# Kernel optimization log

Hardware: AMD Instinct MI355X
Metric: run time of the kernel (lower is better)

## Reference

```python
import jax, jax.numpy as jnp
import numpy as np

# dims
B, CIN, COUT, H, W, K = 4, 64, 64, 128, 128, 9
DM, DS, DC, DI, DTR = K, 16, 4, 2 * K, 1  # mamba: d_model, d_state, d_conv, d_inner, dt_rank=ceil(9/16)
EXTEND_SCOPE = 1.0


def silu(x):
    return x * jax.nn.sigmoid(x)


def conv2d(x, w, b, stride, pad):
    y = jax.lax.conv_general_dilated(x, w, stride, pad, dimension_numbers=("NCHW", "OIHW", "NCHW"))
    return y + b[None, :, None, None]


def group_norm(x, g, b, groups, eps=1e-5):
    Bb, C, Hh, Ww = x.shape
    xg = x.reshape(Bb, groups, C // groups, Hh, Ww)
    mu = xg.mean(axis=(2, 3, 4), keepdims=True)
    var = ((xg - mu) ** 2).mean(axis=(2, 3, 4), keepdims=True)
    xn = ((xg - mu) * jax.lax.rsqrt(var + eps)).reshape(Bb, C, Hh, Ww)
    return xn * g[None, :, None, None] + b[None, :, None, None]


def trc_flatten(x):
    # two-row columnwise interleave flatten; [B,C,Hh,Ww] -> [B,C,Hh*Ww] (Hh even here)
    Bb, Cc, Hh, Ww = x.shape
    return x.reshape(Bb, Cc, Hh // 2, 2, Ww).transpose(0, 1, 2, 4, 3).reshape(Bb, Cc, Hh * Ww)


def trc_inverse(xf, Hh, Ww):
    Bb, Cc, _ = xf.shape
    return xf.reshape(Bb, Cc, Hh // 2, Ww, 2).transpose(0, 1, 2, 4, 3).reshape(Bb, Cc, Hh, Ww)


def mamba(xs, in_proj_w, conv1d_w, conv1d_b, x_proj_w, dt_proj_w, dt_proj_b, A_log, D_p, out_proj_w):
    # standard selective-scan Mamba block; xs: [B,L,DM]
    Bb, L, _ = xs.shape
    xz = xs @ in_proj_w.T                      # [B,L,2*DI]
    xi, z = jnp.split(xz, 2, axis=-1)
    xc = jnp.pad(xi.transpose(0, 2, 1), ((0, 0), (0, 0), (DC - 1, 0)))  # causal pad
    xc = jax.lax.conv_general_dilated(xc, conv1d_w, (1,), "VALID", feature_group_count=DI,
                                      dimension_numbers=("NCH", "OIH", "NCH")) + conv1d_b[None, :, None]
    xi = silu(xc.transpose(0, 2, 1))           # [B,L,DI]
    dbl = xi @ x_proj_w.T
    dt = dbl[..., :DTR]
    Bs = dbl[..., DTR:DTR + DS]
    Cs = dbl[..., DTR + DS:]
    dt = jax.nn.softplus(dt @ dt_proj_w.T + dt_proj_b)  # [B,L,DI]
    A = -jnp.exp(A_log)                        # [DI,DS]
    dA = jnp.exp(dt[..., None] * A)            # [B,L,DI,DS]
    dBx = dt[..., None] * Bs[:, :, None, :] * xi[..., None]

    def step(h, inp):
        da, dbx, c = inp
        h = da * h + dbx
        return h, jnp.einsum("bds,bs->bd", h, c)

    h0 = jnp.zeros((Bb, DI, DS), xs.dtype)
    _, ys = jax.lax.scan(step, h0, (dA.transpose(1, 0, 2, 3), dBx.transpose(1, 0, 2, 3), Cs.transpose(1, 0, 2)))
    y = ys.transpose(1, 0, 2) + D_p * xi
    y = y * silu(z)
    return y @ out_proj_w.T


def bilinear_sample(feat, py, px):
    # feat [B,C,Hf,Wf]; py,px pixel coords [B,Ho,Wo] (already clamped in-range)
    Hf, Wf = feat.shape[-2:]
    y0 = jnp.floor(py)
    x0 = jnp.floor(px)
    wy = (py - y0)[:, None]
    wx = (px - x0)[:, None]
    y0i = jnp.clip(y0.astype(jnp.int32), 0, Hf - 1)
    y1i = jnp.clip(y0i + 1, 0, Hf - 1)
    x0i = jnp.clip(x0.astype(jnp.int32), 0, Wf - 1)
    x1i = jnp.clip(x0i + 1, 0, Wf - 1)
    g = jax.vmap(lambda f, yi, xi: f[:, yi, xi])
    v00 = g(feat, y0i, x0i)
    v01 = g(feat, y0i, x1i)
    v10 = g(feat, y1i, x0i)
    v11 = g(feat, y1i, x1i)
    return v00 * (1 - wy) * (1 - wx) + v01 * (1 - wy) * wx + v10 * wy * (1 - wx) + v11 * wy * wx


def setup_inputs() -> dict:
    key = jax.random.key(0)
    ks = jax.random.split(key, 20)
    r = lambda i, shape, s: jax.random.normal(ks[i], shape, dtype=jnp.float32) * s
    return {
        "x": jax.random.normal(ks[0], (B, CIN, H, W), dtype=jnp.float32),
        "offset_w": r(1, (2 * K, CIN, 3, 3), 0.05),
        "offset_b": jnp.zeros((2 * K,), jnp.float32),
        "gno_g": jnp.ones((2 * K,), jnp.float32),
        "gno_b": jnp.zeros((2 * K,), jnp.float32),
        "altho": jnp.array(np.log(np.e - 1.0), jnp.float32),
        "in_proj_w": r(2, (2 * DI, DM), 0.2),
        "conv1d_w": r(3, (DI, 1, DC), 0.2),
        "conv1d_b": jnp.zeros((DI,), jnp.float32),
        "x_proj_w": r(4, (DTR + 2 * DS, DI), 0.2),
        "dt_proj_w": r(5, (DI, DTR), 0.2),
        "dt_proj_b": r(6, (DI,), 0.2),
        "A_log": jnp.log(jnp.broadcast_to(jnp.arange(1, DS + 1, dtype=jnp.float32), (DI, DS))),
        "D_p": jnp.ones((DI,), jnp.float32),
        "out_proj_w": r(7, (DM, DI), 0.2),
        "dsc_w": r(8, (COUT, CIN, K, 1), 0.05),
        "dsc_b": jnp.zeros((COUT,), jnp.float32),
        "gn_g": jnp.ones((COUT,), jnp.float32),
        "gn_b": jnp.zeros((COUT,), jnp.float32),
    }


def reference(x, offset_w, offset_b, gno_g, gno_b, altho, in_proj_w, conv1d_w, conv1d_b,
              x_proj_w, dt_proj_w, dt_proj_b, A_log, D_p, out_proj_w, dsc_w, dsc_b, gn_g, gn_b):
    off = conv2d(x, offset_w, offset_b, (1, 1), [(1, 1), (1, 1)])      # [B,2K,W,H]
    off = jnp.tanh(group_norm(off, gno_g, gno_b, K))
    y_off = off[:, :K]                                                  # [B,K,W,H]
    center = K // 2
    Wc, Hc = y_off.shape[2], y_off.shape[3]

    # sequential offset accumulation away from the center row (center stays 0)
    rows = [None] * K
    rows[center] = jnp.zeros_like(y_off[:, 0])
    for i in range(1, center + 1):
        rows[center + i] = rows[center + i - 1] + y_off[:, center + i]
        rows[center - i] = rows[center - i + 1] + y_off[:, center - i]
    y_cum = jnp.stack(rows, axis=1)                                     # [B,K,W,H]

    y_center = jnp.arange(Wc, dtype=jnp.float32)[None, None, :, None]
    x_center = jnp.arange(Hc, dtype=jnp.float32)[None, None, None, :]
    x_spread = jnp.linspace(-center, center, K, dtype=jnp.float32)[None, :, None, None]
    y_new = y_center + y_cum * EXTEND_SCOPE                             # y_spread is zeros
    x_new = jnp.broadcast_to(x_center + x_spread, (B, K, Wc, Hc))

    # Mamba selective scan over the two-row columnwise flattened offsets
    y_seq = trc_flatten(y_off).transpose(0, 2, 1)                       # [B, Wc*Hc, K]
    y_m = mamba(y_seq, in_proj_w, conv1d_w, conv1d_b, x_proj_w, dt_proj_w, dt_proj_b, A_log, D_p, out_proj_w)
    y_keep = trc_inverse(y_m.transpose(0, 2, 1), Wc, Hc)                # [B,K,W,H]

    wgt = jnp.maximum(jax.nn.softplus(altho), 0.01)
    y = wgt * y_keep + y_new

    y_map = y.transpose(0, 2, 1, 3).reshape(B, Wc * K, Hc)              # b (w k) h
    x_map = x_new.transpose(0, 2, 1, 3).reshape(B, Wc * K, Hc)

    py = jnp.clip(y_map, 0.0, H - 1)
    px = jnp.clip(x_map, 0.0, W - 1)
    deformed = bilinear_sample(x, py, px)                               # [B,CIN,W*K,H]

    out = conv2d(deformed, dsc_w, dsc_b, (K, 1), "VALID")               # [B,COUT,W,H]
    out = group_norm(out, gn_g, gn_b, COUT // 4)
    return out
```

## Files before the change

### kernel.cpp

```cpp
#include <hip/hip_runtime.h>
#include <math.h>

#define BB 4
#define HH 128
#define WW 128
#define HW (HH*WW)
#define LSEQ HW
#define NCH 1024
#define CLEN 16

typedef _Float16 half8 __attribute__((ext_vector_type(8)));
typedef float floatx4 __attribute__((ext_vector_type(4)));
typedef float floatx16 __attribute__((ext_vector_type(16)));

constexpr size_t OFF_RAW_O = 0;
constexpr size_t OFF_RAW_N = (size_t)BB*10*HW;
constexpr size_t YSEQT_O = OFF_RAW_O + OFF_RAW_N;
constexpr size_t YSEQT_N = (size_t)BB*9*LSEQ;
constexpr size_t YNEW_O = YSEQT_O + YSEQT_N;
constexpr size_t YNEW_N = (size_t)BB*9*HW;
constexpr size_t GN1_O = YNEW_O + YNEW_N;
constexpr size_t GN1_N = 64;
constexpr size_t CH18 = (size_t)BB*18*LSEQ;
constexpr size_t CH16 = (size_t)BB*16*LSEQ;
constexpr size_t DT_O = GN1_O + GN1_N;
constexpr size_t XI_O = DT_O + CH18;
constexpr size_t ZZ_O = XI_O + CH18;
constexpr size_t BS_O = ZZ_O + CH18;
constexpr size_t CS_O = BS_O + CH16;
constexpr size_t CARR = (size_t)BB*NCH*288;
constexpr size_t CP_O = CS_O + CH16;
constexpr size_t CHC_O = CP_O + CARR;
constexpr size_t HIN_O = CHC_O + CARR;
constexpr size_t YS_O = HIN_O + CARR;
constexpr size_t YFIN_O = YS_O + CH18;
constexpr size_t XTH_O = YFIN_O + YNEW_N;
constexpr size_t XTH_N = (size_t)BB*HW*32;
constexpr size_t XTL_O = XTH_O + XTH_N;
constexpr size_t OUTPRE_O = XTL_O + XTH_N;
constexpr size_t OUTPRE_N = (size_t)BB*64*HW;
constexpr size_t WT_O = OUTPRE_O + OUTPRE_N;
constexpr size_t AO_O = WT_O + 36864;
constexpr size_t AMAT_O = AO_O + 9216;
constexpr size_t GN2_O = AMAT_O + 288;
constexpr size_t WS_TOTAL = GN2_O + 128;

__global__ void prep_kernel(const float* __restrict__ dsc_w, const float* __restrict__ offw,
                            const float* __restrict__ A_log,
                            _Float16* __restrict__ AH, _Float16* __restrict__ AL,
                            _Float16* __restrict__ AOH, _Float16* __restrict__ AOL,
                            float* __restrict__ Amat,
                            float* __restrict__ gn1s, float* __restrict__ gn2s){
  int i = blockIdx.x*blockDim.x + threadIdx.x;
  if(blockIdx.x==0){
    if(threadIdx.x<40) gn1s[threadIdx.x]=0.f;
    if(threadIdx.x>=64 && threadIdx.x<192) gn2s[threadIdx.x-64]=0.f;
  }
  if(i < 36864){
    int jj = i&7, gg = (i>>3)&1, co = (i>>4)&63, ks = i>>10;
    int k = ks>>2, q = ks&3;
    int ci = q*16 + gg*8 + jj;
    float w = dsc_w[((size_t)(co*64 + ci))*9 + k];
    _Float16 h = (_Float16)w;
    AH[i] = h;
    AL[i] = (_Float16)(w - (float)h);
  }
  int j = i - 36864;
  if(j >= 0 && j < 9216){
    int jj = j&7, lane = (j>>3)&63, ksl = j>>9;
    int tap = ksl>>1, ks = ksl&1;
    int co = lane&15, kg = lane>>4;
    int ci = ks*32 + kg*8 + jj;
    int dy = tap/3, dx = tap%3;
    float w = (co<10) ? offw[((size_t)(co*64 + ci)*3 + dy)*3 + dx] : 0.f;
    _Float16 h = (_Float16)w;
    AOH[j] = h;
    AOL[j] = (_Float16)(w - (float)h);
  }
  int a = i - 46080;
  if(a >= 0 && a < 288) Amat[a] = -__expf(A_log[a]);
}

__global__ __launch_bounds__(256) void transpose_x_kernel(const float* __restrict__ x,
                                                          _Float16* __restrict__ xTh,
                                                          _Float16* __restrict__ xTl){
  __shared__ float tile[64][65];
  int blk = blockIdx.x;
  int w0 = (blk&1)*64;
  int h  = (blk>>1)&127;
  int b  = blk>>8;
  int lane = threadIdx.x&63, q = threadIdx.x>>6;
  #pragma unroll
  for(int r=0;r<16;r++){
    int ci = r*4 + q;
    tile[ci][lane] = x[((size_t)(b*64+ci)*HH + h)*WW + w0 + lane];
  }
  __syncthreads();
  #pragma unroll
  for(int r=0;r<16;r++){
    int w = r*4 + q;
    float v = tile[lane][w];
    size_t o = (((size_t)(b*HH+h))*WW + w0 + w)*64 + lane;
    _Float16 hv = (_Float16)v;
    xTh[o] = hv;
    xTl[o] = (_Float16)(v - (float)hv);
  }
}

__global__ __launch_bounds__(256) void off_conv_kernel(
    const _Float16* __restrict__ xTh,
    const _Float16* __restrict__ AOH, const _Float16* __restrict__ AOL,
    const float* __restrict__ offb, float* __restrict__ off_raw,
    float* __restrict__ gn1sums){
  __shared__ float sred[6][2];
  int blk0 = blockIdx.x;
  int blk = (blk0&7)*64 + (blk0>>3);
  int h = blk&127, b = blk>>7;
  int lane = threadIdx.x&63, wv = threadIdx.x>>6;
  int col = lane&15, kg = lane>>4;
  if(threadIdx.x<10) ((float*)sred)[threadIdx.x]=0.f;
  __syncthreads();
  floatx4 acc[2];
  acc[0] = (floatx4)0.f; acc[1] = (floatx4)0.f;
  for(int dy=0; dy<3; dy++){
    int hr = h + dy - 1;
    if(hr < 0 || hr >= HH) continue;
    for(int dx=0; dx<3; dx++){
      int tap = dy*3 + dx;
      #pragma unroll
      for(int ks=0; ks<2; ks++){
        half8 ah = *(const half8*)(AOH + (size_t)((tap*2+ks)*64 + lane)*8);
        half8 al = *(const half8*)(AOL + (size_t)((tap*2+ks)*64 + lane)*8);
        #pragma unroll
        for(int tt=0; tt<2; tt++){
          int px = wv*32 + tt*16 + col;
          int wc = px + dx - 1;
          half8 bh = {};
          if(wc >= 0 && wc < WW)
            bh = *(const half8*)(xTh + (((size_t)(b*HH+hr))*WW + wc)*64 + ks*32 + kg*8);
          acc[tt] = __builtin_amdgcn_mfma_f32_16x16x32_f16(ah, bh, acc[tt], 0,0,0);
          acc[tt] = __builtin_amdgcn_mfma_f32_16x16x32_f16(al, bh, acc[tt], 0,0,0);
        }
      }
    }
  }
  float gs[2][2] = {{0.f,0.f},{0.f,0.f}};
  #pragma unroll
  for(int tt=0; tt<2; tt++){
    #pragma unroll
    for(int r=0; r<4; r++){
      int co = kg*4 + r;
      if(co < 10){
        int px = wv*32 + tt*16 + col;
        float v = acc[tt][r] + offb[co];
        off_raw[((size_t)(b*10+co)*HH + h)*WW + px] = v;
        gs[r>>1][0] += v; gs[r>>1][1] += v*v;
      }
    }
  }
  #pragma unroll
  for(int m=1;m<16;m<<=1){
    gs[0][0]+=__shfl_xor(gs[0][0],m,16); gs[0][1]+=__shfl_xor(gs[0][1],m,16);
    gs[1][0]+=__shfl_xor(gs[1][0],m,16); gs[1][1]+=__shfl_xor(gs[1][1],m,16);
  }
  if((lane&15)==0){
    int g0 = kg*2;
    if(g0<5){ atomicAdd(&sred[g0][0],gs[0][0]); atomicAdd(&sred[g0][1],gs[0][1]); }
    if(g0+1<5){ atomicAdd(&sred[g0+1][0],gs[1][0]); atomicAdd(&sred[g0+1][1],gs[1][1]); }
  }
  __syncthreads();
  if(threadIdx.x<10) atomicAdd(&gn1sums[b*10+threadIdx.x], ((float*)sred)[threadIdx.x]);
}

__global__ __launch_bounds__(256) void gn1_apply_kernel(const float* __restrict__ off_raw,
                                                        const float* __restrict__ gn1sums,
                                                        const float* __restrict__ gno_g,
                                                        const float* __restrict__ gno_b,
                                                        float* __restrict__ yseqT,
                                                        float* __restrict__ ynew){
  int idx = blockIdx.x*blockDim.x + threadIdx.x;
  int b = idx>>14; int pix = idx&16383; int h = pix>>7, w = pix&127;
  float t[9];
  #pragma unroll
  for(int c=0;c<9;c++){
    float v = off_raw[((size_t)(b*10+c))*HW + pix];
    int gi = b*10 + (c>>1)*2;
    float S = gn1sums[gi], S2 = gn1sums[gi+1];
    float mu = S*(1.f/32768.f);
    float inv = rsqrtf(S2*(1.f/32768.f) - mu*mu + 1e-5f);
    float xx = (v-mu)*inv*gno_g[c] + gno_b[c];
    xx = fminf(fmaxf(xx,-15.f),15.f);
    float e2 = __expf(2.f*xx);
    t[c] = (e2-1.f)/(e2+1.f);
  }
  int l = (((h>>1)*WW + w)<<1) | (h&1);
  #pragma unroll
  for(int c=0;c<9;c++) yseqT[((size_t)(b*9+c))*LSEQ + l] = t[c];
  float rows[9];
  rows[4]=0.f;
  rows[5]=t[5]; rows[6]=rows[5]+t[6]; rows[7]=rows[6]+t[7]; rows[8]=rows[7]+t[8];
  rows[3]=t[3]; rows[2]=rows[3]+t[2]; rows[1]=rows[2]+t[1]; rows[0]=rows[1]+t[0];
  #pragma unroll
  for(int k=0;k<9;k++) ynew[((size_t)(b*9+k))*HW + pix] = (float)h + rows[k];
}

__global__ __launch_bounds__(256) void mamba_feat_kernel(
    const float* __restrict__ yseqT, const float* __restrict__ in_proj_w,
    const float* __restrict__ conv_w, const float* __restrict__ conv_b,
    const float* __restrict__ x_proj_w, const float* __restrict__ dt_w,
    const float* __restrict__ dt_b,
    float* __restrict__ DT_L, float* __restrict__ XI_L, float* __restrict__ ZZ_L,
    float* __restrict__ BS_L, float* __restrict__ CS_L){
  __shared__ float s_in[36*9], s_cw[18*4], s_cb[18], s_xw[33*18], s_dw[18], s_db[18];
  for(int i=threadIdx.x;i<324;i+=256) s_in[i]=in_proj_w[i];
  for(int i=threadIdx.x;i<72;i+=256)  s_cw[i]=conv_w[i];
  for(int i=threadIdx.x;i<594;i+=256) s_xw[i]=x_proj_w[i];
  if(threadIdx.x<18){ s_cb[threadIdx.x]=conv_b[threadIdx.x];
                      s_dw[threadIdx.x]=dt_w[threadIdx.x];
                      s_db[threadIdx.x]=dt_b[threadIdx.x]; }
  __syncthreads();
  int idx = blockIdx.x*blockDim.x + threadIdx.x;
  int b = idx>>14, l = idx&16383;
  float ys4[4][9];
  #pragma unroll
  for(int m=0;m<9;m++){
    const float* p = yseqT + (size_t)(b*9+m)*LSEQ;
    #pragma unroll
    for(int t=0;t<4;t++){
      int lp = l-3+t;
      ys4[t][m] = (lp>=0) ? p[lp] : 0.f;
    }
  }
  float xi[18];
  #pragma unroll
  for(int d=0;d<18;d++){
    float cacc = s_cb[d];
    #pragma unroll
    for(int t=0;t<4;t++){
      float xr = 0.f;
      #pragma unroll
      for(int m=0;m<9;m++) xr += ys4[t][m]*s_in[d*9+m];
      cacc += xr * s_cw[d*4+t];
    }
    xi[d] = cacc / (1.f + __expf(-cacc));
  }
  float dblv[33];
  #pragma unroll
  for(int j=0;j<33;j++){
    float a=0.f;
    #pragma unroll
    for(int d=0;d<18;d++) a += xi[d]*s_xw[j*18+d];
    dblv[j]=a;
  }
  size_t lb = (size_t)b*LSEQ + l;
  #pragma unroll
  for(int d=0;d<18;d++) XI_L[lb*18 + d] = xi[d];
  #pragma unroll
  for(int d=0;d<18;d++){
    float a=0.f;
    #pragma unroll
    for(int m=0;m<9;m++) a += ys4[3][m]*s_in[(18+d)*9+m];
    ZZ_L[lb*18 + d] = a;
    float pre = dblv[0]*s_dw[d] + s_db[d];
    DT_L[lb*18 + d] = fmaxf(pre,0.f) + __logf(1.f + __expf(-fabsf(pre)));
  }
  #pragma unroll
  for(int s=0;s<16;s++){
    BS_L[lb*16 + s] = dblv[1+s];
    CS_L[lb*16 + s] = dblv[17+s];
  }
}

__global__ __launch_bounds__(288) void scan_pass1(const float* __restrict__ DT_L,
                                                  const float* __restrict__ XI_L,
                                                  const float* __restrict__ BS_L,
                                                  const float* __restrict__ Amat,
                                                  float* __restrict__ CP, float* __restrict__ CH){
  __shared__ float tile[16][18][17];
  int blk = blockIdx.x;
  int b = blk>>6; int ckb = (blk&63)<<4;
  int tid = threadIdx.x;
  int d = tid%18, ck = tid/18;
  int c = ckb + ck;
  int l0 = c*CLEN;
  float A[16];
  #pragma unroll
  for(int i=0;i<4;i++){
    float4 t = *(const float4*)(Amat + d*16 + i*4);
    A[i*4]=t.x; A[i*4+1]=t.y; A[i*4+2]=t.z; A[i*4+3]=t.w;
  }
  float h[16], P[16];
  #pragma unroll
  for(int s=0;s<16;s++){ h[s]=0.f; P[s]=1.f; }
  const float* dtp = DT_L + ((size_t)b*LSEQ + l0)*18 + d;
  const float* xip = XI_L + ((size_t)b*LSEQ + l0)*18 + d;
  const float* bsp = BS_L + ((size_t)b*LSEQ + l0)*16;
  #pragma unroll 4
  for(int st=0; st<CLEN; ++st){
    float dt  = dtp[st*18];
    float dx  = dt*xip[st*18];
    float Bv[16];
    #pragma unroll
    for(int i=0;i<4;i++){
      float4 t = *(const float4*)(bsp + st*16 + i*4);
      Bv[i*4]=t.x; Bv[i*4+1]=t.y; Bv[i*4+2]=t.z; Bv[i*4+3]=t.w;
    }
    #pragma unroll
    for(int s=0;s<16;s++){
      float a = __expf(dt*A[s]);
      h[s] = a*h[s] + dx*Bv[s];
      P[s] *= a;
    }
  }
  #pragma unroll
  for(int s=0;s<16;s++) tile[s][d][ck] = P[s];
  __syncthreads();
  {
    int t = tid; int d2 = t>>4, s2 = t&15;
    float* dst = CP + ((size_t)(b*288 + t))*NCH + ckb;
    const float* src = &tile[s2][d2][0];
    #pragma unroll
    for(int i=0;i<4;i++) ((float4*)dst)[i] = *(const float4*)(src + i*4);
  }
  __syncthreads();
  #pragma unroll
  for(int s=0;s<16;s++) tile[s][d][ck] = h[s];
  __syncthreads();
  {
    int t = tid; int d2 = t>>4, s2 = t&15;
    float* dst = CH + ((size_t)(b*288 + t))*NCH + ckb;
    const float* src = &tile[s2][d2][0];
    #pragma unroll
    for(int i=0;i<4;i++) ((float4*)dst)[i] = *(const float4*)(src + i*4);
  }
}

__global__ __launch_bounds__(256) void scan_carry_kernel(const float* __restrict__ CP,
                                                         const float* __restrict__ CH,
                                                         float* __restrict__ HIN){
  int wid = blockIdx.x*4 + (threadIdx.x>>6);
  int lane = threadIdx.x&63;
  int b = wid/288, t = wid%288;
  size_t base = ((size_t)(b*288 + t))*NCH;
  int c0 = lane*16;
  float P[16], Hh[16];
  #pragma unroll
  for(int i=0;i<4;i++){
    float4 tp = *(const float4*)(CP + base + c0 + i*4);
    float4 th = *(const float4*)(CH + base + c0 + i*4);
    P[i*4]=tp.x; P[i*4+1]=tp.y; P[i*4+2]=tp.z; P[i*4+3]=tp.w;
    Hh[i*4]=th.x; Hh[i*4+1]=th.y; Hh[i*4+2]=th.z; Hh[i*4+3]=th.w;
  }
  float aP = P[0], aH = Hh[0];
  #pragma unroll
  for(int i=1;i<16;i++){ aH = P[i]*aH + Hh[i]; aP = aP*P[i]; }
  float sP = aP, sH = aH;
  #pragma unroll
  for(int off=1; off<64; off<<=1){
    float pP = __shfl_up(sP, off, 64);
    float pH = __shfl_up(sH, off, 64);
    if(lane >= off){ sH = sP*pH + sH; sP = pP*sP; }
  }
  float eH = __shfl_up(sH, 1, 64);
  if(lane==0){ eH=0.f; }
  float cHh = eH;
  float outv[16];
  #pragma unroll
  for(int i=0;i<16;i++){
    outv[i] = cHh;
    cHh = P[i]*cHh + Hh[i];
  }
  #pragma unroll
  for(int i=0;i<4;i++){
    float4 tv; tv.x=outv[i*4]; tv.y=outv[i*4+1]; tv.z=outv[i*4+2]; tv.w=outv[i*4+3];
    *(float4*)(HIN + base + c0 + i*4) = tv;
  }
}

__global__ __launch_bounds__(288) void scan_pass2(const float* __restrict__ DT_L,
                                                  const float* __restrict__ XI_L,
                                                  const float* __restrict__ BS_L,
                                                  const float* __restrict__ CS_L,
                                                  const float* __restrict__ Amat,
                                                  const float* __restrict__ HIN,
                                                  float* __restrict__ YST_L){
  __shared__ float tile[16][18][17];
  int blk = blockIdx.x;
  int b = blk>>6; int ckb = (blk&63)<<4;
  int tid = threadIdx.x;
  int d = tid%18, ck = tid/18;
  int c = ckb + ck;
  int l0 = c*CLEN;
  {
    int t = tid; int d2 = t>>4, s2 = t&15;
    const float* src = HIN + ((size_t)(b*288 + t))*NCH + ckb;
    float* dst = &tile[s2][d2][0];
    #pragma unroll
    for(int i=0;i<4;i++) *(float4*)(dst + i*4) = ((const float4*)src)[i];
  }
  __syncthreads();
  float A[16];
  #pragma unroll
  for(int i=0;i<4;i++){
    float4 t = *(const float4*)(Amat + d*16 + i*4);
    A[i*4]=t.x; A[i*4+1]=t.y; A[i*4+2]=t.z; A[i*4+3]=t.w;
  }
  float h[16];
  #pragma unroll
  for(int s=0;s<16;s++) h[s] = tile[s][d][ck];
  const float* dtp = DT_L + ((size_t)b*LSEQ + l0)*18 + d;
  const float* xip = XI_L + ((size_t)b*LSEQ + l0)*18 + d;
  const float* bsp = BS_L + ((size_t)b*LSEQ + l0)*16;
  const float* csp = CS_L + ((size_t)b*LSEQ + l0)*16;
  float* ysp = YST_L + ((size_t)b*LSEQ + l0)*18 + d;
  #pragma unroll 4
  for(int st=0; st<CLEN; ++st){
    float dt  = dtp[st*18];
    float dx  = dt*xip[st*18];
    float Bv[16], Cv[16];
    #pragma unroll
    for(int i=0;i<4;i++){
      float4 t = *(const float4*)(bsp + st*16 + i*4);
      Bv[i*4]=t.x; Bv[i*4+1]=t.y; Bv[i*4+2]=t.z; Bv[i*4+3]=t.w;
      float4 u = *(const float4*)(csp + st*16 + i*4);
      Cv[i*4]=u.x; Cv[i*4+1]=u.y; Cv[i*4+2]=u.z; Cv[i*4+3]=u.w;
    }
    float pc = 0.f;
    #pragma unroll
    for(int s=0;s<16;s++){
      float a = __expf(dt*A[s]);
      h[s] = a*h[s] + dx*Bv[s];
      pc += h[s]*Cv[s];
    }
    ysp[st*18] = pc;
  }
}

__global__ __launch_bounds__(256) void mamba_out_kernel(
    const float* __restrict__ YST_L, const float* __restrict__ XI_L,
    const float* __restrict__ ZZ_L, const float* __restrict__ Dp,
    const float* __restrict__ out_w, const float* __restrict__ altho,
    const float* __restrict__ ynew, float* __restrict__ yfin){
  __shared__ float s_ow[9*18], s_dp[18];
  for(int i=threadIdx.x;i<162;i+=256) s_ow[i]=out_w[i];
  if(threadIdx.x<18) s_dp[threadIdx.x]=Dp[threadIdx.x];
  __syncthreads();
  int idx = blockIdx.x*blockDim.x + threadIdx.x;
  int b = idx>>14, l = idx&16383;
  size_t lb = (size_t)b*LSEQ + l;
  float y[18];
  #pragma unroll
  for(int d=0;d<18;d++){
    float z = ZZ_L[lb*18+d];
    float sz = z/(1.f+__expf(-z));
    y[d] = (YST_L[lb*18+d] + s_dp[d]*XI_L[lb*18+d]) * sz;
  }
  float av = altho[0];
  float sp = fmaxf(av,0.f)+__logf(1.f+__expf(-fabsf(av)));
  float wgt = fmaxf(sp, 0.01f);
  int h = ((l>>8)<<1) | (l&1);
  int w = (l>>1)&127;
  int pix = h*WW + w;
  #pragma unroll
  for(int m=0;m<9;m++){
    float a=0.f;
    #pragma unroll
    for(int d=0;d<18;d++) a += y[d]*s_ow[m*18+d];
    size_t o = ((size_t)(b*9+m))*HW + pix;
    yfin[o] = wgt*a + ynew[o];
  }
}

__global__ __launch_bounds__(256) void sample_conv_kernel(
    const _Float16* __restrict__ xTh, const float* __restrict__ yfin,
    const _Float16* __restrict__ AH, const _Float16* __restrict__ AL,
    const float* __restrict__ bias, float* __restrict__ outpre,
    float* __restrict__ gn2sums){
  __shared__ _Float16 F[2][64][72];
  __shared__ float sred2[16][2];
  int blk0 = blockIdx.x;
  int blk = (blk0&7)*128 + (blk0>>3);
  int wo0 = (blk&1)*64;
  int ho  = (blk>>1)&127;
  int b   = blk>>8;
  int lane = threadIdx.x&63;
  int wv   = threadIdx.x>>6;
  int l32  = lane&31, g = lane>>5;
  int co0 = (wv&1)*32, pxh = (wv>>1)*32;
  int px = lane;
  int wo = wo0 + px;
  if(threadIdx.x<32) ((float*)sred2)[threadIdx.x]=0.f;

  const _Float16* ahbase = AH + ((size_t)(co0 + l32)*2 + g)*8;
  const _Float16* albase = AL + ((size_t)(co0 + l32)*2 + g)*8;

  floatx16 acc;
  #pragma unroll
  for(int r=0;r<16;r++) acc[r]=0.f;

  half8 h0[2], h1[2]; _Float16 wyh = (_Float16)0.f;
  auto gather = [&](int k){
    float yv = yfin[((size_t)(b*9+k))*HW + ho*WW + wo];
    float py = fminf(fmaxf(yv,0.f),127.f);
    float y0f = floorf(py);
    wyh = (_Float16)(py - y0f);
    int iy0 = (int)y0f;
    int iy1 = min(iy0+1,127);
    int xc  = min(max(wo + k - 4, 0), 127);
    size_t o0 = (((size_t)(b*HH+iy0))*WW + xc)*64 + wv*16;
    size_t o1 = (((size_t)(b*HH+iy1))*WW + xc)*64 + wv*16;
    h0[0] = *(const half8*)(xTh + o0);
    h0[1] = *(const half8*)(xTh + o0 + 8);
    h1[0] = *(const half8*)(xTh + o1);
    h1[1] = *(const half8*)(xTh + o1 + 8);
  };
  auto writeF = [&](int buf){
    half8 w8 = {wyh,wyh,wyh,wyh,wyh,wyh,wyh,wyh};
    #pragma unroll
    for(int q=0;q<2;q++){
      half8 r = h0[q] + (h1[q]-h0[q])*w8;
      *(half8*)&F[buf][px][wv*16 + q*8] = r;
    }
  };

  gather(0); writeF(0);
  __syncthreads();
  #pragma unroll
  for(int k=0;k<9;k++){
    if(k<8) gather(k+1);
    int buf = k&1;
    #pragma unroll
    for(int q=0;q<4;q++){
      half8 bh = *(const half8*)&F[buf][pxh + l32][q*16 + g*8];
      half8 ah = *(const half8*)(ahbase + (size_t)(k*4+q)*1024);
      half8 al = *(const half8*)(albase + (size_t)(k*4+q)*1024);
      acc = __builtin_amdgcn_mfma_f32_32x32x16_f16(ah, bh, acc, 0,0,0);
      acc = __builtin_amdgcn_mfma_f32_32x32x16_f16(al, bh, acc, 0,0,0);
    }
    if(k<8) writeF((k+1)&1);
    __syncthreads();
  }
  float qs[4][2] = {{0,0},{0,0},{0,0},{0,0}};
  #pragma unroll
  for(int r=0;r<16;r++){
    int row = (r&3) + 8*(r>>2) + 4*g;
    int co = co0 + row;
    float v = acc[r] + bias[co];
    outpre[((size_t)(b*64+co))*HW + ho*WW + wo0 + pxh + l32] = v;
    qs[r>>2][0] += v; qs[r>>2][1] += v*v;
  }
  #pragma unroll
  for(int qi=0;qi<4;qi++){
    int gq = (co0>>2) + 2*qi + g;
    atomicAdd(&sred2[gq][0], qs[qi][0]);
    atomicAdd(&sred2[gq][1], qs[qi][1]);
  }
  __syncthreads();
  if(threadIdx.x<32) atomicAdd(&gn2sums[b*32+threadIdx.x], ((float*)sred2)[threadIdx.x]);
}

__global__ __launch_bounds__(256) void gn2_apply_kernel(const float* __restrict__ src,
                                                        const float* __restrict__ gn2sums,
                                                        const float* __restrict__ gam,
                                                        const float* __restrict__ bet,
                                                        float* __restrict__ dst){
  int idx = blockIdx.x*blockDim.x + threadIdx.x;
  int c = (idx>>14)&63;
  int b = idx>>20;
  int gi = b*32 + (c>>2)*2;
  float S = gn2sums[gi], S2 = gn2sums[gi+1];
  float mu = S*(1.f/65536.f);
  float inv = rsqrtf(S2*(1.f/65536.f) - mu*mu + 1e-5f);
  dst[idx] = (src[idx]-mu)*inv*gam[c] + bet[c];
}

extern "C" void kernel_launch(void* const* d_in, const int* in_sizes, int n_in,
                              void* d_out, int out_size, void* d_ws, size_t ws_size,
                              hipStream_t stream){
  const float* x        = (const float*)d_in[0];
  const float* offset_w = (const float*)d_in[1];
  const float* offset_b = (const float*)d_in[2];
  const float* gno_g    = (const float*)d_in[3];
  const float* gno_b    = (const float*)d_in[4];
  const float* altho    = (const float*)d_in[5];
  const float* in_proj  = (const float*)d_in[6];
  const float* conv1d_w = (const float*)d_in[7];
  const float* conv1d_b = (const float*)d_in[8];
  const float* x_proj   = (const float*)d_in[9];
  const float* dt_w     = (const float*)d_in[10];
  const float* dt_b     = (const float*)d_in[11];
  const float* A_log    = (const float*)d_in[12];
  const float* D_p      = (const float*)d_in[13];
  const float* out_proj = (const float*)d_in[14];
  const float* dsc_w    = (const float*)d_in[15];
  const float* dsc_b    = (const float*)d_in[16];
  const float* gn_g     = (const float*)d_in[17];
  const float* gn_b     = (const float*)d_in[18];
  float* out = (float*)d_out;
  float* ws  = (float*)d_ws;
  if(ws_size < WS_TOTAL*sizeof(float)) return;

  float* off_raw = ws + OFF_RAW_O;
  float* yseqT   = ws + YSEQT_O;
  float* ynew    = ws + YNEW_O;
  float* gn1s    = ws + GN1_O;
  float* DT_L    = ws + DT_O;
  float* XI_L    = ws + XI_O;
  float* ZZ_L    = ws + ZZ_O;
  float* BS_L    = ws + BS_O;
  float* CS_L    = ws + CS_O;
  float* CP      = ws + CP_O;
  float* CH      = ws + CHC_O;
  float* HIN     = ws + HIN_O;
  float* YST_L   = ws + YS_O;
  float* yfin    = ws + YFIN_O;
  _Float16* xTh  = (_Float16*)(ws + XTH_O);
  _Float16* xTl  = (_Float16*)(ws + XTL_O);
  float* outpre  = ws + OUTPRE_O;
  _Float16* AH   = (_Float16*)(ws + WT_O);
  _Float16* AL   = (_Float16*)(ws + WT_O) + 36864;
  _Float16* AOH  = (_Float16*)(ws + AO_O);
  _Float16* AOL  = (_Float16*)(ws + AO_O) + 9216;
  float* Amat    = ws + AMAT_O;
  float* gn2s    = ws + GN2_O;

  prep_kernel<<<dim3(182), dim3(256), 0, stream>>>(dsc_w, offset_w, A_log, AH, AL, AOH, AOL,
                                                   Amat, gn1s, gn2s);
  transpose_x_kernel<<<dim3(1024), dim3(256), 0, stream>>>(x, xTh, xTl);
  off_conv_kernel<<<dim3(512), dim3(256), 0, stream>>>(xTh, AOH, AOL, offset_b, off_raw, gn1s);
  gn1_apply_kernel<<<dim3(256), dim3(256), 0, stream>>>(off_raw, gn1s, gno_g, gno_b, yseqT, ynew);
  mamba_feat_kernel<<<dim3(256), dim3(256), 0, stream>>>(yseqT, in_proj, conv1d_w, conv1d_b,
                                                         x_proj, dt_w, dt_b,
                                                         DT_L, XI_L, ZZ_L, BS_L, CS_L);
  scan_pass1<<<dim3(BB*NCH/16), dim3(288), 0, stream>>>(DT_L, XI_L, BS_L, Amat, CP, CH);
  scan_carry_kernel<<<dim3(288), dim3(256), 0, stream>>>(CP, CH, HIN);
  scan_pass2<<<dim3(BB*NCH/16), dim3(288), 0, stream>>>(DT_L, XI_L, BS_L, CS_L, Amat, HIN, YST_L);
  mamba_out_kernel<<<dim3(256), dim3(256), 0, stream>>>(YST_L, XI_L, ZZ_L, D_p, out_proj, altho,
                                                        ynew, yfin);
  sample_conv_kernel<<<dim3(1024), dim3(256), 0, stream>>>(xTh, yfin, AH, AL, dsc_b, outpre, gn2s);
  gn2_apply_kernel<<<dim3(16384), dim3(256), 0, stream>>>(outpre, gn2s, gn_g, gn_b, out);
}
```

Baseline: 241.0 us.

## Stage conv rows in LDS, coalesce mamba I/O, deepen sample pipeline, drop xTl

Several independent changes. The offset conv now stages each padded input row in shared memory, so taps read from LDS instead of issuing repeated global loads. The mamba feature and output kernels route their per-position 18- and 16-wide vectors through shared memory, turning strided per-thread accesses into coalesced float4 transfers. The sampling conv prefetches yfin once, spreads the gathers across all threads in 8-half chunks, and uses a triple-buffered pipeline that issues gathers two steps ahead; the transpose also stops writing the unused low-half copy of x. These add LDS use and barriers that may lower occupancy.

```diff
diff --git a/kernel.cpp b/kernel.cpp
--- a/kernel.cpp
+++ b/kernel.cpp
@@ -82,8 +82,7 @@
 }
 
 __global__ __launch_bounds__(256) void transpose_x_kernel(const float* __restrict__ x,
-                                                          _Float16* __restrict__ xTh,
-                                                          _Float16* __restrict__ xTl){
+                                                          _Float16* __restrict__ xTh){
   __shared__ float tile[64][65];
   int blk = blockIdx.x;
   int w0 = (blk&1)*64;
@@ -100,10 +99,7 @@
   for(int r=0;r<16;r++){
     int w = r*4 + q;
     float v = tile[lane][w];
-    size_t o = (((size_t)(b*HH+h))*WW + w0 + w)*64 + lane;
-    _Float16 hv = (_Float16)v;
-    xTh[o] = hv;
-    xTl[o] = (_Float16)(v - (float)hv);
+    xTh[(((size_t)(b*HH+h))*WW + w0 + w)*64 + lane] = (_Float16)v;
   }
 }
 
@@ -112,19 +108,30 @@
     const _Float16* __restrict__ AOH, const _Float16* __restrict__ AOL,
     const float* __restrict__ offb, float* __restrict__ off_raw,
     float* __restrict__ gn1sums){
+  __shared__ _Float16 R[130][72];
   __shared__ float sred[6][2];
   int blk0 = blockIdx.x;
   int blk = (blk0&7)*64 + (blk0>>3);
   int h = blk&127, b = blk>>7;
-  int lane = threadIdx.x&63, wv = threadIdx.x>>6;
+  int tid = threadIdx.x;
+  int lane = tid&63, wv = tid>>6;
   int col = lane&15, kg = lane>>4;
-  if(threadIdx.x<10) ((float*)sred)[threadIdx.x]=0.f;
-  __syncthreads();
+  int chunk = tid&7, pxg = tid>>3;
+  if(tid<10) ((float*)sred)[tid]=0.f;
   floatx4 acc[2];
   acc[0] = (floatx4)0.f; acc[1] = (floatx4)0.f;
   for(int dy=0; dy<3; dy++){
     int hr = h + dy - 1;
     if(hr < 0 || hr >= HH) continue;
+    __syncthreads();
+    const _Float16* rowp = xTh + ((size_t)(b*HH+hr))*WW*64 + chunk*8;
+    for(int px = pxg; px < 130; px += 32){
+      int wc = px - 1;
+      half8 v = {};
+      if(wc >= 0 && wc < WW) v = *(const half8*)(rowp + (size_t)wc*64);
+      *(half8*)&R[px][chunk*8] = v;
+    }
+    __syncthreads();
     for(int dx=0; dx<3; dx++){
       int tap = dy*3 + dx;
       #pragma unroll
@@ -134,10 +141,7 @@
         #pragma unroll
         for(int tt=0; tt<2; tt++){
           int px = wv*32 + tt*16 + col;
-          int wc = px + dx - 1;
-          half8 bh = {};
-          if(wc >= 0 && wc < WW)
-            bh = *(const half8*)(xTh + (((size_t)(b*HH+hr))*WW + wc)*64 + ks*32 + kg*8);
+          half8 bh = *(const half8*)&R[px+dx][ks*32 + kg*8];
           acc[tt] = __builtin_amdgcn_mfma_f32_16x16x32_f16(ah, bh, acc[tt], 0,0,0);
           acc[tt] = __builtin_amdgcn_mfma_f32_16x16x32_f16(al, bh, acc[tt], 0,0,0);
         }
@@ -169,7 +173,7 @@
     if(g0+1<5){ atomicAdd(&sred[g0+1][0],gs[1][0]); atomicAdd(&sred[g0+1][1],gs[1][1]); }
   }
   __syncthreads();
-  if(threadIdx.x<10) atomicAdd(&gn1sums[b*10+threadIdx.x], ((float*)sred)[threadIdx.x]);
+  if(tid<10) atomicAdd(&gn1sums[b*10+tid], ((float*)sred)[tid]);
 }
 
 __global__ __launch_bounds__(256) void gn1_apply_kernel(const float* __restrict__ off_raw,
@@ -212,6 +216,7 @@
     float* __restrict__ DT_L, float* __restrict__ XI_L, float* __restrict__ ZZ_L,
     float* __restrict__ BS_L, float* __restrict__ CS_L){
   __shared__ float s_in[36*9], s_cw[18*4], s_cb[18], s_xw[33*18], s_dw[18], s_db[18];
+  __shared__ float buf[256*18];
   for(int i=threadIdx.x;i<324;i+=256) s_in[i]=in_proj_w[i];
   for(int i=threadIdx.x;i<72;i+=256)  s_cw[i]=conv_w[i];
   for(int i=threadIdx.x;i<594;i+=256) s_xw[i]=x_proj_w[i];
@@ -219,8 +224,10 @@
                       s_dw[threadIdx.x]=dt_w[threadIdx.x];
                       s_db[threadIdx.x]=dt_b[threadIdx.x]; }
   __syncthreads();
-  int idx = blockIdx.x*blockDim.x + threadIdx.x;
+  int tid = threadIdx.x;
+  int idx = blockIdx.x*256 + tid;
   int b = idx>>14, l = idx&16383;
+  int l0 = (blockIdx.x*256)&16383;
   float ys4[4][9];
   #pragma unroll
   for(int m=0;m<9;m++){
@@ -252,23 +259,41 @@
     for(int d=0;d<18;d++) a += xi[d]*s_xw[j*18+d];
     dblv[j]=a;
   }
-  size_t lb = (size_t)b*LSEQ + l;
-  #pragma unroll
-  for(int d=0;d<18;d++) XI_L[lb*18 + d] = xi[d];
+  float zz[18], dtv[18];
   #pragma unroll
   for(int d=0;d<18;d++){
     float a=0.f;
     #pragma unroll
     for(int m=0;m<9;m++) a += ys4[3][m]*s_in[(18+d)*9+m];
-    ZZ_L[lb*18 + d] = a;
+    zz[d] = a;
     float pre = dblv[0]*s_dw[d] + s_db[d];
-    DT_L[lb*18 + d] = fmaxf(pre,0.f) + __logf(1.f + __expf(-fabsf(pre)));
-  }
-  #pragma unroll
-  for(int s=0;s<16;s++){
-    BS_L[lb*16 + s] = dblv[1+s];
-    CS_L[lb*16 + s] = dblv[17+s];
-  }
+    dtv[d] = fmaxf(pre,0.f) + __logf(1.f + __expf(-fabsf(pre)));
+  }
+  auto dump18 = [&](const float* v, float* gbase){
+    #pragma unroll
+    for(int d=0;d<18;d++) buf[tid*18+d] = v[d];
+    __syncthreads();
+    float4* gp = (float4*)gbase;
+    const float4* lp = (const float4*)buf;
+    for(int j=tid; j<1152; j+=256) gp[j] = lp[j];
+    __syncthreads();
+  };
+  size_t base18 = ((size_t)b*LSEQ + l0)*18;
+  dump18(xi,  XI_L + base18);
+  dump18(zz,  ZZ_L + base18);
+  dump18(dtv, DT_L + base18);
+  auto dump16 = [&](const float* v, float* gbase){
+    #pragma unroll
+    for(int s=0;s<16;s++) buf[tid*16+s] = v[s];
+    __syncthreads();
+    float4* gp = (float4*)gbase;
+    const float4* lp = (const float4*)buf;
+    for(int j=tid; j<1024; j+=256) gp[j] = lp[j];
+    __syncthreads();
+  };
+  size_t base16 = ((size_t)b*LSEQ + l0)*16;
+  dump16(dblv+1,  BS_L + base16);
+  dump16(dblv+17, CS_L + base16);
 }
 
 __global__ __launch_bounds__(288) void scan_pass1(const float* __restrict__ DT_L,
@@ -442,18 +467,32 @@
     const float* __restrict__ out_w, const float* __restrict__ altho,
     const float* __restrict__ ynew, float* __restrict__ yfin){
   __shared__ float s_ow[9*18], s_dp[18];
+  __shared__ float buf[256*18];
   for(int i=threadIdx.x;i<162;i+=256) s_ow[i]=out_w[i];
   if(threadIdx.x<18) s_dp[threadIdx.x]=Dp[threadIdx.x];
-  __syncthreads();
-  int idx = blockIdx.x*blockDim.x + threadIdx.x;
+  int tid = threadIdx.x;
+  int idx = blockIdx.x*256 + tid;
   int b = idx>>14, l = idx&16383;
-  size_t lb = (size_t)b*LSEQ + l;
+  int l0 = (blockIdx.x*256)&16383;
+  size_t base18 = ((size_t)b*LSEQ + l0)*18;
+  auto load18 = [&](const float* gbase, float* v){
+    __syncthreads();
+    float4* lp = (float4*)buf;
+    const float4* gp = (const float4*)gbase;
+    for(int j=tid; j<1152; j+=256) lp[j] = gp[j];
+    __syncthreads();
+    #pragma unroll
+    for(int d=0;d<18;d++) v[d] = buf[tid*18+d];
+  };
+  float yst[18], xi[18], zz[18];
+  load18(YST_L + base18, yst);
+  load18(XI_L + base18, xi);
+  load18(ZZ_L + base18, zz);
   float y[18];
   #pragma unroll
   for(int d=0;d<18;d++){
-    float z = ZZ_L[lb*18+d];
-    float sz = z/(1.f+__expf(-z));
-    y[d] = (YST_L[lb*18+d] + s_dp[d]*XI_L[lb*18+d]) * sz;
+    float sz = zz[d]/(1.f+__expf(-zz[d]));
+    y[d] = (yst[d] + s_dp[d]*xi[d]) * sz;
   }
   float av = altho[0];
   float sp = fmaxf(av,0.f)+__logf(1.f+__expf(-fabsf(av)));
@@ -476,21 +515,28 @@
     const _Float16* __restrict__ AH, const _Float16* __restrict__ AL,
     const float* __restrict__ bias, float* __restrict__ outpre,
     float* __restrict__ gn2sums){
-  __shared__ _Float16 F[2][64][72];
+  __shared__ _Float16 F[3][64][72];
   __shared__ float sred2[16][2];
   int blk0 = blockIdx.x;
   int blk = (blk0&7)*128 + (blk0>>3);
   int wo0 = (blk&1)*64;
   int ho  = (blk>>1)&127;
   int b   = blk>>8;
-  int lane = threadIdx.x&63;
-  int wv   = threadIdx.x>>6;
+  int tid = threadIdx.x;
+  int lane = tid&63;
+  int wv   = tid>>6;
   int l32  = lane&31, g = lane>>5;
   int co0 = (wv&1)*32, pxh = (wv>>1)*32;
-  int px = lane;
-  int wo = wo0 + px;
-  if(threadIdx.x<32) ((float*)sred2)[threadIdx.x]=0.f;
-
+  if(tid<32) ((float*)sred2)[tid]=0.f;
+
+  int pxsub = tid>>3, chunk = tid&7;
+  float yv[2][9];
+  #pragma unroll
+  for(int r=0;r<2;r++){
+    const float* yp = yfin + (size_t)b*9*HW + ho*WW + wo0 + r*32 + pxsub;
+    #pragma unroll
+    for(int k=0;k<9;k++) yv[r][k] = yp[(size_t)k*HW];
+  }
   const _Float16* ahbase = AH + ((size_t)(co0 + l32)*2 + g)*8;
   const _Float16* albase = AL + ((size_t)(co0 + l32)*2 + g)*8;
 
@@ -498,47 +544,58 @@
   #pragma unroll
   for(int r=0;r<16;r++) acc[r]=0.f;
 
-  half8 h0[2], h1[2]; _Float16 wyh = (_Float16)0.f;
-  auto gather = [&](int k){
-    float yv = yfin[((size_t)(b*9+k))*HW + ho*WW + wo];
-    float py = fminf(fmaxf(yv,0.f),127.f);
-    float y0f = floorf(py);
-    wyh = (_Float16)(py - y0f);
-    int iy0 = (int)y0f;
-    int iy1 = min(iy0+1,127);
-    int xc  = min(max(wo + k - 4, 0), 127);
-    size_t o0 = (((size_t)(b*HH+iy0))*WW + xc)*64 + wv*16;
-    size_t o1 = (((size_t)(b*HH+iy1))*WW + xc)*64 + wv*16;
-    h0[0] = *(const half8*)(xTh + o0);
-    h0[1] = *(const half8*)(xTh + o0 + 8);
-    h1[0] = *(const half8*)(xTh + o1);
-    h1[1] = *(const half8*)(xTh + o1 + 8);
+  auto issue = [&](int k, half8* s0, half8* s1){
+    #pragma unroll
+    for(int r=0;r<2;r++){
+      int px = r*32 + pxsub;
+      float py = fminf(fmaxf(yv[r][k],0.f),127.f);
+      int iy0 = (int)py;
+      int iy1 = min(iy0+1,127);
+      int xc = min(max(wo0 + px + k - 4, 0), 127);
+      const _Float16* p0 = xTh + (((size_t)(b*HH+iy0))*WW + xc)*64 + chunk*8;
+      const _Float16* p1 = xTh + (((size_t)(b*HH+iy1))*WW + xc)*64 + chunk*8;
+      s0[r] = *(const half8*)p0;
+      s1[r] = *(const half8*)p1;
+    }
   };
-  auto writeF = [&](int buf){
-    half8 w8 = {wyh,wyh,wyh,wyh,wyh,wyh,wyh,wyh};
-    #pragma unroll
-    for(int q=0;q<2;q++){
-      half8 r = h0[q] + (h1[q]-h0[q])*w8;
-      *(half8*)&F[buf][px][wv*16 + q*8] = r;
+  auto writeF = [&](int k, int buf, const half8* s0, const half8* s1){
+    #pragma unroll
+    for(int r=0;r<2;r++){
+      int px = r*32 + pxsub;
+      float py = fminf(fmaxf(yv[r][k],0.f),127.f);
+      _Float16 wy = (_Float16)(py - floorf(py));
+      half8 w8 = {wy,wy,wy,wy,wy,wy,wy,wy};
+      half8 res = s0[r] + (s1[r]-s0[r])*w8;
+      *(half8*)&F[buf][px][chunk*8] = res;
     }
   };
 
-  gather(0); writeF(0);
+  half8 sA0[2], sA1[2], sB0[2], sB1[2];
+  issue(0, sA0, sA1);
+  issue(1, sB0, sB1);
+  writeF(0, 0, sA0, sA1);
   __syncthreads();
   #pragma unroll
   for(int k=0;k<9;k++){
-    if(k<8) gather(k+1);
-    int buf = k&1;
+    half8 ahk[4], alk[4];
     #pragma unroll
     for(int q=0;q<4;q++){
-      half8 bh = *(const half8*)&F[buf][pxh + l32][q*16 + g*8];
-      half8 ah = *(const half8*)(ahbase + (size_t)(k*4+q)*1024);
-      half8 al = *(const half8*)(albase + (size_t)(k*4+q)*1024);
-      acc = __builtin_amdgcn_mfma_f32_32x32x16_f16(ah, bh, acc, 0,0,0);
-      acc = __builtin_amdgcn_mfma_f32_32x32x16_f16(al, bh, acc, 0,0,0);
-    }
-    if(k<8) writeF((k+1)&1);
-    __syncthreads();
+      ahk[q] = *(const half8*)(ahbase + (size_t)(k*4+q)*1024);
+      alk[q] = *(const half8*)(albase + (size_t)(k*4+q)*1024);
+    }
+    if(k<7) issue(k+2, sA0, sA1);
+    if(k<8) writeF(k+1, (k+1)%3, sB0, sB1);
+    __syncthreads();
+    #pragma unroll
+    for(int q=0;q<4;q++){
+      half8 bh = *(const half8*)&F[k%3][pxh + l32][q*16 + g*8];
+      acc = __builtin_amdgcn_mfma_f32_32x32x16_f16(ahk[q], bh, acc, 0,0,0);
+      acc = __builtin_amdgcn_mfma_f32_32x32x16_f16(alk[q], bh, acc, 0,0,0);
+    }
+    if(k<7){
+      #pragma unroll
+      for(int r=0;r<2;r++){ sB0[r]=sA0[r]; sB1[r]=sA1[r]; }
+    }
   }
   float qs[4][2] = {{0,0},{0,0},{0,0},{0,0}};
   #pragma unroll
@@ -556,7 +613,7 @@
     atomicAdd(&sred2[gq][1], qs[qi][1]);
   }
   __syncthreads();
-  if(threadIdx.x<32) atomicAdd(&gn2sums[b*32+threadIdx.x], ((float*)sred2)[threadIdx.x]);
+  if(tid<32) atomicAdd(&gn2sums[b*32+tid], ((float*)sred2)[tid]);
 }
 
 __global__ __launch_bounds__(256) void gn2_apply_kernel(const float* __restrict__ src,
@@ -615,7 +672,6 @@
   float* YST_L   = ws + YS_O;
   float* yfin    = ws + YFIN_O;
   _Float16* xTh  = (_Float16*)(ws + XTH_O);
-  _Float16* xTl  = (_Float16*)(ws + XTL_O);
   float* outpre  = ws + OUTPRE_O;
   _Float16* AH   = (_Float16*)(ws + WT_O);
   _Float16* AL   = (_Float16*)(ws + WT_O) + 36864;
@@ -626,7 +682,7 @@
 
   prep_kernel<<<dim3(182), dim3(256), 0, stream>>>(dsc_w, offset_w, A_log, AH, AL, AOH, AOL,
                                                    Amat, gn1s, gn2s);
-  transpose_x_kernel<<<dim3(1024), dim3(256), 0, stream>>>(x, xTh, xTl);
+  transpose_x_kernel<<<dim3(1024), dim3(256), 0, stream>>>(x, xTh);
   off_conv_kernel<<<dim3(512), dim3(256), 0, stream>>>(xTh, AOH, AOL, offset_b, off_raw, gn1s);
   gn1_apply_kernel<<<dim3(256), dim3(256), 0, stream>>>(off_raw, gn1s, gno_g, gno_b, yseqT, ynew);
   mamba_feat_kernel<<<dim3(256), dim3(256), 0, stream>>>(yseqT, in_proj, conv1d_w, conv1d_b,
```

Measured after the change: 255.3 us. +5.9%, slower.
